# Performance work log

Hardware: AMD Instinct MI355X
Metric: run time of the kernel (lower is better)

## Reference

```python
import jax, jax.numpy as jnp
import numpy as np

TAU = 1.5
SCALE = 0.125
EPS = 1e-5
H = 8

@jax.custom_vjp
def spike(u):
    return (u >= 0.0).astype(u.dtype)

def _spike_fwd(u):
    return spike(u), u

def _spike_bwd(u, g):
    # ATan surrogate gradient, alpha=2 (spikingjelly default)
    return (g / (1.0 + (jnp.pi * u) ** 2),)

spike.defvjp(_spike_fwd, _spike_bwd)

def lif_ms(xt):
    # xt: (T, ...) multi-step LIF, decay_input=True, v_th=1, hard reset to 0, detach_reset
    def step(v, x):
        v = v + (x - v) / TAU
        s = spike(v - 1.0)
        v = v * (1.0 - jax.lax.stop_gradient(s))
        return v, s
    _, s = jax.lax.scan(step, jnp.zeros_like(xt[0]), xt)
    return s

def bn(x, g, b, m, var):
    # eval-mode BatchNorm1d over channel dim of (B, C, L)
    inv = g / jnp.sqrt(var + EPS)
    return (x - m[None, :, None]) * inv[None, :, None] + b[None, :, None]

def setup_inputs() -> dict:
    key = jax.random.key(0)
    ks = jax.random.split(key, 16)
    B, C, T, N = 8, 512, 4, 256
    w_scale = 1.0 / np.sqrt(C)
    inp = {
        'x': jax.random.normal(ks[0], (B, C, T, N), jnp.float32),
        'wq': jax.random.normal(ks[1], (C, C), jnp.float32) * w_scale,
        'wk': jax.random.normal(ks[2], (C, C), jnp.float32) * w_scale,
        'wv': jax.random.normal(ks[3], (C, C), jnp.float32) * w_scale,
        'wp': jax.random.normal(ks[4], (C, C), jnp.float32) * w_scale,
        'bp': jnp.zeros((C,), jnp.float32),
        'gq': jax.random.uniform(ks[5], (C,), jnp.float32, 0.5, 1.5),
        'bq': jax.random.uniform(ks[6], (C,), jnp.float32),
        'mq': jnp.zeros((C,), jnp.float32),
        'vq': jnp.ones((C,), jnp.float32),
        'gk': jax.random.uniform(ks[7], (C,), jnp.float32, 0.5, 1.5),
        'bk': jax.random.uniform(ks[8], (C,), jnp.float32),
        'mk': jnp.zeros((C,), jnp.float32),
        'vk': jnp.ones((C,), jnp.float32),
        'gv': jax.random.uniform(ks[9], (C,), jnp.float32, 0.5, 1.5),
        'bv': jax.random.uniform(ks[10], (C,), jnp.float32),
        'mv': jnp.zeros((C,), jnp.float32),
        'vv': jnp.ones((C,), jnp.float32),
        'gp': jax.random.uniform(ks[11], (C,), jnp.float32, 0.5, 1.5),
        'bpn': jax.random.uniform(ks[12], (C,), jnp.float32),
        'mp': jnp.zeros((C,), jnp.float32),
        'vp': jnp.ones((C,), jnp.float32),
    }
    return inp

def reference(x, wq, wk, wv, wp, bp, gq, bq, mq, vq, gk, bk, mk, vk,
              gv, bv, mv, vv, gp, bpn, mp, vp):
    B, C, T, N = x.shape
    L = T * N
    d = C // H

    # proj_bn then multi-step proj_lif over time dim
    xb = bn(x.reshape(B, C, L), gp, bpn, mp, vp).reshape(B, C, T, N)
    s0 = lif_ms(jnp.transpose(xb, (2, 0, 1, 3)))            # (T,B,C,N)
    x_for_qkv = jnp.transpose(s0, (1, 2, 0, 3)).reshape(B, C, L)  # (B,C,L)

    def qkv_branch(w, g, b_, m, v_):
        y = bn(jnp.einsum('oc,bcl->bol', w, x_for_qkv), g, b_, m, v_)
        y = y.reshape(B, C, T, N)
        sy = lif_ms(jnp.transpose(y, (2, 0, 1, 3)))         # (T,B,C,N)
        sy = jnp.transpose(sy, (1, 0, 3, 2)).reshape(B, L, C)  # (B,T,N,C)->(B,L,C)
        return jnp.transpose(sy.reshape(B, L, H, d), (0, 2, 1, 3))  # (B,H,L,d)

    q = qkv_branch(wq, gq, bq, mq, vq)
    k = qkv_branch(wk, gk, bk, mk, vk)
    v = qkv_branch(wv, gv, bv, mv, vv)

    attn = jnp.einsum('bhqd,bhkd->bhqk', q, k)              # no softmax
    o = jnp.einsum('bhqk,bhkd->bhqd', attn, v) * SCALE
    o = jnp.transpose(o, (0, 1, 3, 2)).reshape(B, C, L)

    # single-step attn_lif: v = o/tau from zero state, spike at threshold 1
    s = spike(o / TAU - 1.0)

    out = jnp.einsum('oc,bcl->bol', wp, s) + bp[None, :, None]
    return out.reshape(B, C, T, N)
```

## Files before the change

### kernel.cpp

```cpp
#include <hip/hip_runtime.h>
#include <hip/hip_bf16.h>


#define NB 8
#define NC 512
#define NT 4
#define NN 256
#define NL 1024
#define NH 8
#define ND 64
#define BCL (NB*NC*NL)

typedef __attribute__((ext_vector_type(8))) short  short8v;
typedef __attribute__((ext_vector_type(8))) unsigned short us8;
typedef __attribute__((ext_vector_type(4))) unsigned short us4;
typedef __attribute__((ext_vector_type(4))) float f32x4;

__device__ __forceinline__ float bu2f(unsigned short u) {
  return __uint_as_float(((unsigned)u) << 16);
}
__device__ __forceinline__ unsigned short f2bu(float f) {
  unsigned b = __float_as_uint(f);
  return (unsigned short)((b + 0x7FFFu + ((b >> 16) & 1u)) >> 16);
}

__global__ void k_prep(const float* __restrict__ wq, const float* __restrict__ wk,
                       const float* __restrict__ wv, const float* __restrict__ wp,
                       const float* __restrict__ x,
                       const float* __restrict__ g,  const float* __restrict__ bt,
                       const float* __restrict__ mu, const float* __restrict__ var,
                       unsigned short* __restrict__ H2,
                       unsigned short* __restrict__ ST0) {
  if (blockIdx.x < 512) {
    int gi = blockIdx.x * 256 + threadIdx.x;
    int p = gi >> 15;
    int o = (gi >> 6) & 511;
    int k8 = gi & 63;
    int rt = o >> 7, r = o & 127;
    int k0i = k8 >> 3, chunk = k8 & 7;
    const float* W = (p == 0) ? wq : (p == 1) ? wk : (p == 2) ? wv : wp;
    const float* src = W + (size_t)o * NC + k8 * 8;
    us8 a[3];
#pragma unroll
    for (int i = 0; i < 8; i++) {
      float w = src[i];
      unsigned short u1 = f2bu(w);
      float r1 = w - bu2f(u1);
      unsigned short u2 = f2bu(r1);
      float r2 = r1 - bu2f(u2);
      unsigned short u3 = f2bu(r2);
      a[0][i] = u1; a[1][i] = u2; a[2][i] = u3;
    }
#pragma unroll
    for (int j = 0; j < 3; j++) {
      size_t off = ((size_t)((((p * 3 + j) * 4 + rt) * 8 + k0i) * 8 + chunk)) * 1024
                   + (size_t)r * 8;
      *(us8*)&H2[off] = a[j];
    }
  } else {
    int bidx = blockIdx.x - 512;
    int b  = bidx >> 6;
    int c0 = (bidx & 63) * 8;
    int n  = threadIdx.x;
    unsigned short spk[NT][8];
#pragma unroll
    for (int i = 0; i < 8; i++) {
      int c = c0 + i;
      float inv = g[c] / sqrtf(var[c] + 1e-5f);
      float m = mu[c], be = bt[c];
      const float* xp = x + ((size_t)(b * NC + c)) * NL + n;
      float v = 0.f;
#pragma unroll
      for (int t = 0; t < NT; t++) {
        float y = (xp[t * NN] - m) * inv + be;
        v = v + (y - v) / 1.5f;
        unsigned short s = 0;
        if (v - 1.0f >= 0.f) { s = 0x3F80; v = 0.f; }
        spk[t][i] = s;
      }
    }
#pragma unroll
    for (int t = 0; t < NT; t++) {
      us8 pk;
#pragma unroll
      for (int i = 0; i < 8; i++) pk[i] = spk[t][i];
      *(us8*)&ST0[((size_t)b * NL + t * NN + n) * NC + c0] = pk;
    }
  }
}

__global__ __launch_bounds__(256) void
k_qkv(const unsigned short* __restrict__ H2,
      const unsigned short* __restrict__ ST0,
      const float* __restrict__ gq, const float* __restrict__ bq,
      const float* __restrict__ mq, const float* __restrict__ vq,
      const float* __restrict__ gk, const float* __restrict__ bk,
      const float* __restrict__ mk, const float* __restrict__ vk,
      const float* __restrict__ gv, const float* __restrict__ bv,
      const float* __restrict__ mv, const float* __restrict__ vv,
      unsigned short* __restrict__ STq, unsigned short* __restrict__ STkT,
      unsigned short* __restrict__ STvT) {
  __shared__ __align__(16) unsigned short sB[2][128 * 64];

  int id = blockIdx.x;
  int xcd = id & 7, slot = id >> 3;
  int b = xcd;
  int grp = slot >> 3;
  int p = grp >> 2, rt = grp & 3;
  int n0 = (slot & 7) * 32;

  int tid = threadIdx.x;
  int w = tid >> 6, lane = tid & 63, quad = lane >> 4, l15 = lane & 15;
  int xorv = l15 & 7;

  const unsigned short* Sb = ST0 + (size_t)b * NL * NC;
  const unsigned short* Hbase = H2 + ((size_t)((p * 3) * 4 + rt) * 8) * 8192;

  f32x4 acc[2][8];
#pragma unroll
  for (int ri = 0; ri < 2; ri++)
#pragma unroll
    for (int jj = 0; jj < 8; jj++) acc[ri][jj] = (f32x4){0.f, 0.f, 0.f, 0.f};

  short8v A0[2][3][2], A1[2][3][2];

#define QLOADA(DST, K0I)                                                     \
  _Pragma("unroll") for (int ks = 0; ks < 2; ks++) {                         \
    int c8 = ks * 4 + quad;                                                  \
    _Pragma("unroll") for (int j = 0; j < 3; j++) {                          \
      const unsigned short* Hj =                                             \
          Hbase + ((size_t)(j * 4 * 8 + (K0I))) * 8192 + (size_t)c8 * 1024;  \
      DST[ks][j][0] = *(const short8v*)&Hj[(w * 32 + l15) * 8];              \
      DST[ks][j][1] = *(const short8v*)&Hj[(w * 32 + 16 + l15) * 8];         \
    }                                                                        \
  }

  QLOADA(A0, 0);

  us8 breg[4];
  int ccs[4], segs[4];
  size_t bsrc[4];
#pragma unroll
  for (int i = 0; i < 4; i++) {
    int idx = tid + i * 256;
    int cc = idx >> 3, seg = idx & 7;
    int t = (cc >> 4) & 3, nn = (cc & 15) | ((cc >> 6) << 4);
    ccs[i] = cc; segs[i] = seg;
    bsrc[i] = (size_t)(t * NN + n0 + nn) * NC + seg * 8;
  }
#pragma unroll
  for (int i = 0; i < 4; i++) breg[i] = *(const us8*)&Sb[bsrc[i]];
#pragma unroll
  for (int i = 0; i < 4; i++)
    *(us8*)&sB[0][ccs[i] * 64 + ((segs[i] ^ (ccs[i] & 7)) << 3)] = breg[i];

#define QBPRE(K0N)                                                           \
  _Pragma("unroll") for (int i = 0; i < 4; i++)                              \
    breg[i] = *(const us8*)&Sb[bsrc[i] + (size_t)(K0N) * 64];

#define QBWRITE(BUFN)                                                        \
  _Pragma("unroll") for (int i = 0; i < 4; i++)                              \
    *(us8*)&sB[BUFN][ccs[i] * 64 + ((segs[i] ^ (ccs[i] & 7)) << 3)] = breg[i];

#define QMFMAS(AR, BUF)                                                      \
  _Pragma("unroll") for (int ks = 0; ks < 2; ks++) {                         \
    int c8 = ks * 4 + quad;                                                  \
    int poff = (c8 ^ xorv) << 3;                                             \
    short8v bf[8];                                                           \
    _Pragma("unroll") for (int jj = 0; jj < 8; jj++)                         \
      bf[jj] = *(const short8v*)&sB[BUF][(jj * 16 + l15) * 64 + poff];       \
    _Pragma("unroll") for (int j = 0; j < 3; j++)                            \
      _Pragma("unroll") for (int jj = 0; jj < 8; jj++) {                     \
        acc[0][jj] = __builtin_amdgcn_mfma_f32_16x16x32_bf16(                \
            AR[ks][j][0], bf[jj], acc[0][jj], 0, 0, 0);                      \
        acc[1][jj] = __builtin_amdgcn_mfma_f32_16x16x32_bf16(                \
            AR[ks][j][1], bf[jj], acc[1][jj], 0, 0, 0);                      \
      }                                                                      \
  }

#define QSTEP(K0I, ACUR, ANXT)                                               \
  __syncthreads();                                                           \
  { if ((K0I) < 7) { QLOADA(ANXT, (K0I) + 1); } }                            \
  { if ((K0I) < 7) { QBPRE((K0I) + 1); } }                                   \
  QMFMAS(ACUR, (K0I) & 1);                                                   \
  { if ((K0I) < 7) { QBWRITE(((K0I) & 1) ^ 1); } }

  QSTEP(0, A0, A1)
  QSTEP(1, A1, A0)
  QSTEP(2, A0, A1)
  QSTEP(3, A1, A0)
  QSTEP(4, A0, A1)
  QSTEP(5, A1, A0)
  QSTEP(6, A0, A1)
  QSTEP(7, A1, A0)

#undef QLOADA
#undef QBPRE
#undef QBWRITE
#undef QMFMAS
#undef QSTEP

  const float *g, *bb, *mpt, *vr;
  unsigned short* So;
  if (p == 0)      { g = gq; bb = bq; mpt = mq; vr = vq; So = STq; }
  else if (p == 1) { g = gk; bb = bk; mpt = mk; vr = vk; So = STkT; }
  else             { g = gv; bb = bv; mpt = mv; vr = vv; So = STvT; }
  So += (size_t)b * NL * NC;

  unsigned short spa[2][2][4][4];
#pragma unroll
  for (int ri = 0; ri < 2; ri++) {
    int ob = rt * 128 + w * 32 + ri * 16 + quad * 4;
    float av[4], mvv[4], bvv[4];
#pragma unroll
    for (int r = 0; r < 4; r++) {
      av[r]  = g[ob + r] / sqrtf(vr[ob + r] + 1e-5f);
      mvv[r] = mpt[ob + r];
      bvv[r] = bb[ob + r];
    }
#pragma unroll
    for (int nh = 0; nh < 2; nh++) {
#pragma unroll
      for (int r = 0; r < 4; r++) {
        float vmem = 0.f;
#pragma unroll
        for (int t = 0; t < NT; t++) {
          float y = (acc[ri][nh * 4 + t][r] - mvv[r]) * av[r] + bvv[r];
          vmem = vmem + (y - vmem) / 1.5f;
          unsigned short s = 0;
          if (vmem - 1.0f >= 0.f) { s = 0x3F80; vmem = 0.f; }
          spa[ri][nh][t][r] = s;
        }
      }
    }
  }

  __syncthreads();
  unsigned short* sT = &sB[0][0];

  if (p == 0) {
#pragma unroll
    for (int ri = 0; ri < 2; ri++)
#pragma unroll
      for (int nh = 0; nh < 2; nh++)
#pragma unroll
        for (int t = 0; t < 4; t++)
#pragma unroll
          for (int r = 0; r < 4; r++) {
            int lloc = t * 32 + (nh << 4) + l15;
            int col = w * 32 + ri * 16 + quad * 4 + r;
            int ch = col >> 3;
            int pch = (ch & 8) | ((ch & 7) ^ (lloc & 7));
            sT[lloc * 128 + (pch << 3) + (col & 7)] = spa[ri][nh][t][r];
          }
    __syncthreads();
#pragma unroll
    for (int ss = 0; ss < 2; ss++) {
      int s = tid + ss * 256;
      int lloc = s >> 2, seg = s & 3;
      int t = lloc >> 5, nn = lloc & 31;
      size_t rowg = (size_t)(t * NN + n0 + nn) * NC + rt * 128 + seg * 32;
#pragma unroll
      for (int i = 0; i < 4; i++) {
        int ch = seg * 4 + i;
        int pch = (ch & 8) | ((ch & 7) ^ (lloc & 7));
        us8 v = *(const us8*)&sT[lloc * 128 + (pch << 3)];
        *(us8*)&So[rowg + i * 8] = v;
      }
    }
  } else {
#pragma unroll
    for (int ri = 0; ri < 2; ri++)
#pragma unroll
      for (int nh = 0; nh < 2; nh++)
#pragma unroll
        for (int t = 0; t < 4; t++)
#pragma unroll
          for (int r = 0; r < 4; r++) {
            int row = w * 32 + ri * 16 + quad * 4 + r;
            int col = t * 32 + (nh << 4) + l15;
            int phys = (((col >> 3) ^ (row & 7)) << 3) | (col & 7);
            sT[row * 128 + phys] = spa[ri][nh][t][r];
          }
    __syncthreads();
#pragma unroll
    for (int ss = 0; ss < 2; ss++) {
      int s = tid + ss * 256;
      int c = s >> 2, t = s & 3;
#pragma unroll
      for (int i = 0; i < 4; i++) {
        int g8 = t * 4 + i;
        us8 v = *(const us8*)&sT[c * 128 + ((g8 ^ (c & 7)) << 3)];
        *(us8*)&So[(size_t)(rt * 128 + c) * NL + t * 256 + n0 + i * 8] = v;
      }
    }
  }
}

__global__ __launch_bounds__(256) void
k_kvM(const unsigned short* __restrict__ STkT,
      const unsigned short* __restrict__ STvT,
      float* __restrict__ Mpart) {
  int bh = blockIdx.x, ch = blockIdx.y;
  int b = bh >> 3, h = bh & 7;
  const unsigned short* KT = STkT + ((size_t)(b * NC + h * ND)) * NL;
  const unsigned short* VT = STvT + ((size_t)(b * NC + h * ND)) * NL;
  int tid = threadIdx.x;
  int w = tid >> 6, lane = tid & 63, quad = lane >> 4, l15 = lane & 15;
  int lb = ch * 128;

  f32x4 acc[4];
#pragma unroll
  for (int jj = 0; jj < 4; jj++) acc[jj] = (f32x4){0.f, 0.f, 0.f, 0.f};

#pragma unroll
  for (int ks = 0; ks < 4; ks++) {
    int lc = lb + ks * 32 + quad * 8;
    short8v a = *(const short8v*)&KT[(size_t)(w * 16 + l15) * NL + lc];
#pragma unroll
    for (int jj = 0; jj < 4; jj++) {
      short8v bv = *(const short8v*)&VT[(size_t)(jj * 16 + l15) * NL + lc];
      acc[jj] = __builtin_amdgcn_mfma_f32_16x16x32_bf16(a, bv, acc[jj], 0, 0, 0);
    }
  }

  float* Mp = Mpart + ((size_t)ch * 64 + bh) * 4096;
#pragma unroll
  for (int jj = 0; jj < 4; jj++)
#pragma unroll
    for (int r = 0; r < 4; r++)
      Mp[(w * 16 + quad * 4 + r) * ND + jj * 16 + l15] = acc[jj][r];
}

__global__ __launch_bounds__(256) void
k_red(const float* __restrict__ Mpart, float* __restrict__ Msum) {
  int i = blockIdx.x * 256 + threadIdx.x;
  float4 s = ((const float4*)Mpart)[i];
#pragma unroll
  for (int ch = 1; ch < 8; ch++) {
    float4 t = ((const float4*)Mpart)[(size_t)ch * 65536 + i];
    s.x += t.x; s.y += t.y; s.z += t.z; s.w += t.w;
  }
  ((float4*)Msum)[i] = s;
}

__global__ __launch_bounds__(256) void
k_attn(const unsigned short* __restrict__ STq,
       const float* __restrict__ Msum,
       unsigned short* __restrict__ STs) {
  __shared__ unsigned short MT1[64 * 64];
  __shared__ unsigned short MT2[64 * 64];
  __shared__ unsigned short sQ[128 * 64];
  int lt = blockIdx.x, bh = blockIdx.y;
  int b = bh >> 3, h = bh & 7;
  int tid = threadIdx.x;
  int w = tid >> 6, lane = tid & 63, quad = lane >> 4, l15 = lane & 15;

  const unsigned short* Qp = STq + (size_t)b * NL * NC + h * ND;

#pragma unroll
  for (int i = 0; i < 4; i++) {
    int idx = tid + i * 256;
    int row = idx >> 3, c8 = idx & 7;
    us8 v = *(const us8*)&Qp[(size_t)(lt * 128 + row) * NC + c8 * 8];
    *(us8*)&sQ[row * 64 + ((c8 ^ (row & 7)) << 3)] = v;
  }

#pragma unroll
  for (int i = 0; i < 4; i++) {
    int idx4 = tid + i * 256;
    float4 s = ((const float4*)Msum)[(size_t)bh * 1024 + idx4];
    int e = idx4 >> 4;
    int dd0 = (idx4 * 4) & 63;
    int chunk = e >> 3;
    float sv[4] = {s.x, s.y, s.z, s.w};
#pragma unroll
    for (int r = 0; r < 4; r++) {
      int dd = dd0 + r;
      unsigned short u1 = f2bu(sv[r]);
      unsigned short u2 = f2bu(sv[r] - bu2f(u1));
      int pos = dd * 64 + (((chunk ^ (dd & 7)) << 3) | (e & 7));
      MT1[pos] = u1;
      MT2[pos] = u2;
    }
  }
  __syncthreads();

  f32x4 acc[4][2];
#pragma unroll
  for (int dt = 0; dt < 4; dt++)
#pragma unroll
    for (int j = 0; j < 2; j++) acc[dt][j] = (f32x4){0.f, 0.f, 0.f, 0.f};

#pragma unroll
  for (int ks = 0; ks < 2; ks++) {
    short8v bq[2];
#pragma unroll
    for (int ltile = 0; ltile < 2; ltile++) {
      int row = w * 32 + ltile * 16 + l15;
      bq[ltile] = *(const short8v*)&sQ[row * 64
                                       + (((ks * 4 + quad) ^ (row & 7)) << 3)];
    }
    int c8 = ks * 4 + quad;
#pragma unroll
    for (int dt = 0; dt < 4; dt++) {
      int dd = dt * 16 + l15;
      int off = dd * 64 + ((c8 ^ (dd & 7)) << 3);
      short8v a1 = *(const short8v*)&MT1[off];
      short8v a2 = *(const short8v*)&MT2[off];
#pragma unroll
      for (int ltile = 0; ltile < 2; ltile++) {
        acc[dt][ltile] = __builtin_amdgcn_mfma_f32_16x16x32_bf16(a1, bq[ltile], acc[dt][ltile], 0, 0, 0);
        acc[dt][ltile] = __builtin_amdgcn_mfma_f32_16x16x32_bf16(a2, bq[ltile], acc[dt][ltile], 0, 0, 0);
      }
    }
  }

  __syncthreads();
#pragma unroll
  for (int dt = 0; dt < 4; dt++)
#pragma unroll
    for (int ltile = 0; ltile < 2; ltile++) {
      int row = w * 32 + ltile * 16 + l15;
#pragma unroll
      for (int r = 0; r < 4; r++) {
        int col = dt * 16 + quad * 4 + r;
        int phys = (((col >> 3) ^ (row & 7)) << 3) | (col & 7);
        sQ[row * 64 + phys] = (acc[dt][ltile][r] >= 12.0f) ? 0x3F80 : 0;
      }
    }
  __syncthreads();

  unsigned short* Sp = STs + (size_t)b * NL * NC + h * ND;
  {
    int row = tid >> 1, seg = tid & 1;
    size_t dst = (size_t)(lt * 128 + row) * NC + seg * 32;
#pragma unroll
    for (int i = 0; i < 4; i++) {
      int ch = seg * 4 + i;
      us8 v = *(const us8*)&sQ[row * 64 + ((ch ^ (row & 7)) << 3)];
      *(us8*)&Sp[dst + i * 8] = v;
    }
  }
}

__global__ __launch_bounds__(256) void
k_out(const unsigned short* __restrict__ H2,
      const unsigned short* __restrict__ STs,
      const float* __restrict__ bp, float* __restrict__ out) {
  __shared__ __align__(16) unsigned short sB[2][64 * 64];

  int id = blockIdx.x;
  int xcd = id & 7, slot = id >> 3;
  int b  = xcd;
  int rt = slot >> 4;
  int l0 = (slot & 15) * 64;

  int tid = threadIdx.x;
  int w = tid >> 6, lane = tid & 63, quad = lane >> 4, l15 = lane & 15;
  int xorv = l15 & 7;

  const unsigned short* Sb = STs + (size_t)b * NL * NC;
  const unsigned short* Hbase = H2 + ((size_t)(9 * 4 + rt) * 8) * 8192;

  f32x4 acc[2][4];
#pragma unroll
  for (int ri = 0; ri < 2; ri++)
#pragma unroll
    for (int jj = 0; jj < 4; jj++) acc[ri][jj] = (f32x4){0.f, 0.f, 0.f, 0.f};

  short8v A0[2][3][2], A1[2][3][2];

#define OLOADA(DST, K0I)                                                     \
  _Pragma("unroll") for (int ks = 0; ks < 2; ks++) {                         \
    int c8 = ks * 4 + quad;                                                  \
    _Pragma("unroll") for (int j = 0; j < 3; j++) {                          \
      const unsigned short* Hj =                                             \
          Hbase + ((size_t)(j * 4 * 8 + (K0I))) * 8192 + (size_t)c8 * 1024;  \
      DST[ks][j][0] = *(const short8v*)&Hj[(w * 32 + l15) * 8];              \
      DST[ks][j][1] = *(const short8v*)&Hj[(w * 32 + 16 + l15) * 8];         \
    }                                                                        \
  }

  OLOADA(A0, 0);

  us8 breg[2];
  int ccs[2], segs[2];
  size_t bsrc[2];
#pragma unroll
  for (int i = 0; i < 2; i++) {
    int idx = tid + i * 256;
    int cc = idx >> 3, seg = idx & 7;
    ccs[i] = cc; segs[i] = seg;
    bsrc[i] = (size_t)(l0 + cc) * NC + seg * 8;
  }
#pragma unroll
  for (int i = 0; i < 2; i++) breg[i] = *(const us8*)&Sb[bsrc[i]];
#pragma unroll
  for (int i = 0; i < 2; i++)
    *(us8*)&sB[0][ccs[i] * 64 + ((segs[i] ^ (ccs[i] & 7)) << 3)] = breg[i];

#define OBPRE(K0N)                                                           \
  _Pragma("unroll") for (int i = 0; i < 2; i++)                              \
    breg[i] = *(const us8*)&Sb[bsrc[i] + (size_t)(K0N) * 64];

#define OBWRITE(BUFN)                                                        \
  _Pragma("unroll") for (int i = 0; i < 2; i++)                              \
    *(us8*)&sB[BUFN][ccs[i] * 64 + ((segs[i] ^ (ccs[i] & 7)) << 3)] = breg[i];

#define OMFMAS(AR, BUF)                                                      \
  _Pragma("unroll") for (int ks = 0; ks < 2; ks++) {                         \
    int c8 = ks * 4 + quad;                                                  \
    int poff = (c8 ^ xorv) << 3;                                             \
    short8v bf[4];                                                           \
    _Pragma("unroll") for (int jj = 0; jj < 4; jj++)                         \
      bf[jj] = *(const short8v*)&sB[BUF][(jj * 16 + l15) * 64 + poff];       \
    _Pragma("unroll") for (int j = 0; j < 3; j++)                            \
      _Pragma("unroll") for (int jj = 0; jj < 4; jj++) {                     \
        acc[0][jj] = __builtin_amdgcn_mfma_f32_16x16x32_bf16(                \
            AR[ks][j][0], bf[jj], acc[0][jj], 0, 0, 0);                      \
        acc[1][jj] = __builtin_amdgcn_mfma_f32_16x16x32_bf16(                \
            AR[ks][j][1], bf[jj], acc[1][jj], 0, 0, 0);                      \
      }                                                                      \
  }

#define OSTEP(K0I, ACUR, ANXT)                                               \
  __syncthreads();                                                           \
  { if ((K0I) < 7) { OLOADA(ANXT, (K0I) + 1); } }                            \
  { if ((K0I) < 7) { OBPRE((K0I) + 1); } }                                   \
  OMFMAS(ACUR, (K0I) & 1);                                                   \
  { if ((K0I) < 7) { OBWRITE(((K0I) & 1) ^ 1); } }

  OSTEP(0, A0, A1)
  OSTEP(1, A1, A0)
  OSTEP(2, A0, A1)
  OSTEP(3, A1, A0)
  OSTEP(4, A0, A1)
  OSTEP(5, A1, A0)
  OSTEP(6, A0, A1)
  OSTEP(7, A1, A0)

#undef OLOADA
#undef OBPRE
#undef OBWRITE
#undef OMFMAS
#undef OSTEP

#pragma unroll
  for (int ri = 0; ri < 2; ri++) {
    int ob = rt * 128 + w * 32 + ri * 16 + quad * 4;
#pragma unroll
    for (int jj = 0; jj < 4; jj++) {
      int l = l0 + jj * 16 + l15;
#pragma unroll
      for (int r = 0; r < 4; r++)
        out[((size_t)(b * NC + ob + r)) * NL + l] = acc[ri][jj][r] + bp[ob + r];
    }
  }
}

extern "C" void kernel_launch(void* const* d_in, const int* in_sizes, int n_in,
                              void* d_out, int out_size, void* d_ws, size_t ws_size,
                              hipStream_t stream) {
  (void)in_sizes; (void)n_in; (void)out_size; (void)ws_size;
  const float* x   = (const float*)d_in[0];
  const float* wq  = (const float*)d_in[1];
  const float* wk  = (const float*)d_in[2];
  const float* wv  = (const float*)d_in[3];
  const float* wp  = (const float*)d_in[4];
  const float* bp  = (const float*)d_in[5];
  const float* gq  = (const float*)d_in[6];
  const float* bq  = (const float*)d_in[7];
  const float* mq  = (const float*)d_in[8];
  const float* vq  = (const float*)d_in[9];
  const float* gk  = (const float*)d_in[10];
  const float* bk  = (const float*)d_in[11];
  const float* mk  = (const float*)d_in[12];
  const float* vk  = (const float*)d_in[13];
  const float* gv  = (const float*)d_in[14];
  const float* bv  = (const float*)d_in[15];
  const float* mv  = (const float*)d_in[16];
  const float* vvv = (const float*)d_in[17];
  const float* gp  = (const float*)d_in[18];
  const float* bpn = (const float*)d_in[19];
  const float* mp  = (const float*)d_in[20];
  const float* vp  = (const float*)d_in[21];

  unsigned short* H2   = (unsigned short*)d_ws;
  unsigned short* ST0  = H2 + (size_t)4 * 3 * NC * NC;
  unsigned short* STq  = ST0 + BCL;
  unsigned short* STkT = STq + BCL;
  unsigned short* STvT = STkT + BCL;
  unsigned short* STs  = STvT + BCL;
  float* Mpart = (float*)(STs + BCL);
  float* Msum  = Mpart + (size_t)8 * 64 * 4096;

  dim3 blk(256);
  k_prep<<<1024, blk, 0, stream>>>(wq, wk, wv, wp, x, gp, bpn, mp, vp, H2, ST0);
  k_qkv<<<768, blk, 0, stream>>>(H2, ST0,
      gq, bq, mq, vq, gk, bk, mk, vk, gv, bv, mv, vvv, STq, STkT, STvT);
  k_kvM<<<dim3(64, 8), blk, 0, stream>>>(STkT, STvT, Mpart);
  k_red<<<256, blk, 0, stream>>>(Mpart, Msum);
  k_attn<<<dim3(8, 64), blk, 0, stream>>>(STq, Msum, STs);
  k_out<<<512, blk, 0, stream>>>(H2, STs, bp, (float*)d_out);
}
```

Baseline: 182.5 us.

## Replace triple-bf16 weight split with two-term fp16 split in projection GEMMs

Weights are now split into an fp16 high part and a residual scaled by 2^11, instead of three bf16 terms. Spikes are encoded as fp16 ones, and the GEMMs use f16 MFMA. The K loop runs twice, residual term first, with the accumulator rescaled by 2^-11 before the high term is added. This removes a third of the MFMA work and weight loads. It restructures the loop to stream one weight term per pass, which re-reads the B tiles from global memory and LDS twice and doubles the number of barriers. The fp16 range and precision of the split weights could differ slightly from the fp32 reference, which matters near spike thresholds.

```diff
diff --git a/kernel.cpp b/kernel.cpp
--- a/kernel.cpp
+++ b/kernel.cpp
@@ -12,6 +12,7 @@
 #define BCL (NB*NC*NL)
 
 typedef __attribute__((ext_vector_type(8))) short  short8v;
+typedef __attribute__((ext_vector_type(8))) _Float16 h8;
 typedef __attribute__((ext_vector_type(8))) unsigned short us8;
 typedef __attribute__((ext_vector_type(4))) unsigned short us4;
 typedef __attribute__((ext_vector_type(4))) float f32x4;
@@ -40,20 +41,19 @@
     int k0i = k8 >> 3, chunk = k8 & 7;
     const float* W = (p == 0) ? wq : (p == 1) ? wk : (p == 2) ? wv : wp;
     const float* src = W + (size_t)o * NC + k8 * 8;
-    us8 a[3];
+    us8 a[2];
 #pragma unroll
     for (int i = 0; i < 8; i++) {
       float w = src[i];
-      unsigned short u1 = f2bu(w);
-      float r1 = w - bu2f(u1);
-      unsigned short u2 = f2bu(r1);
-      float r2 = r1 - bu2f(u2);
-      unsigned short u3 = f2bu(r2);
-      a[0][i] = u1; a[1][i] = u2; a[2][i] = u3;
-    }
-#pragma unroll
-    for (int j = 0; j < 3; j++) {
-      size_t off = ((size_t)((((p * 3 + j) * 4 + rt) * 8 + k0i) * 8 + chunk)) * 1024
+      _Float16 h1 = (_Float16)w;
+      float r1 = w - (float)h1;
+      _Float16 h2 = (_Float16)(r1 * 2048.0f);
+      a[0][i] = __builtin_bit_cast(unsigned short, h1);
+      a[1][i] = __builtin_bit_cast(unsigned short, h2);
+    }
+#pragma unroll
+    for (int j = 0; j < 2; j++) {
+      size_t off = ((size_t)((((p * 2 + j) * 4 + rt) * 8 + k0i) * 8 + chunk)) * 1024
                    + (size_t)r * 8;
       *(us8*)&H2[off] = a[j];
     }
@@ -75,7 +75,7 @@
         float y = (xp[t * NN] - m) * inv + be;
         v = v + (y - v) / 1.5f;
         unsigned short s = 0;
-        if (v - 1.0f >= 0.f) { s = 0x3F80; v = 0.f; }
+        if (v - 1.0f >= 0.f) { s = 0x3C00; v = 0.f; }
         spk[t][i] = s;
       }
     }
@@ -114,7 +114,7 @@
   int xorv = l15 & 7;
 
   const unsigned short* Sb = ST0 + (size_t)b * NL * NC;
-  const unsigned short* Hbase = H2 + ((size_t)((p * 3) * 4 + rt) * 8) * 8192;
+  const unsigned short* Hbase = H2 + ((size_t)((p * 2) * 4 + rt) * 8) * 8192;
 
   f32x4 acc[2][8];
 #pragma unroll
@@ -122,20 +122,18 @@
 #pragma unroll
     for (int jj = 0; jj < 8; jj++) acc[ri][jj] = (f32x4){0.f, 0.f, 0.f, 0.f};
 
-  short8v A0[2][3][2], A1[2][3][2];
-
-#define QLOADA(DST, K0I)                                                     \
+  h8 A0[2][2], A1[2][2];
+
+#define QLOADA(DST, J, K0I)                                                  \
   _Pragma("unroll") for (int ks = 0; ks < 2; ks++) {                         \
     int c8 = ks * 4 + quad;                                                  \
-    _Pragma("unroll") for (int j = 0; j < 3; j++) {                          \
-      const unsigned short* Hj =                                             \
-          Hbase + ((size_t)(j * 4 * 8 + (K0I))) * 8192 + (size_t)c8 * 1024;  \
-      DST[ks][j][0] = *(const short8v*)&Hj[(w * 32 + l15) * 8];              \
-      DST[ks][j][1] = *(const short8v*)&Hj[(w * 32 + 16 + l15) * 8];         \
-    }                                                                        \
-  }
-
-  QLOADA(A0, 0);
+    const unsigned short* Hj =                                               \
+        Hbase + ((size_t)((J) * 4 * 8 + (K0I))) * 8192 + (size_t)c8 * 1024;  \
+    DST[ks][0] = *(const h8*)&Hj[(w * 32 + l15) * 8];                        \
+    DST[ks][1] = *(const h8*)&Hj[(w * 32 + 16 + l15) * 8];                   \
+  }
+
+  QLOADA(A0, 1, 0);
 
   us8 breg[4];
   int ccs[4], segs[4];
@@ -166,33 +164,44 @@
   _Pragma("unroll") for (int ks = 0; ks < 2; ks++) {                         \
     int c8 = ks * 4 + quad;                                                  \
     int poff = (c8 ^ xorv) << 3;                                             \
-    short8v bf[8];                                                           \
-    _Pragma("unroll") for (int jj = 0; jj < 8; jj++)                         \
-      bf[jj] = *(const short8v*)&sB[BUF][(jj * 16 + l15) * 64 + poff];       \
-    _Pragma("unroll") for (int j = 0; j < 3; j++)                            \
-      _Pragma("unroll") for (int jj = 0; jj < 8; jj++) {                     \
-        acc[0][jj] = __builtin_amdgcn_mfma_f32_16x16x32_bf16(                \
-            AR[ks][j][0], bf[jj], acc[0][jj], 0, 0, 0);                      \
-        acc[1][jj] = __builtin_amdgcn_mfma_f32_16x16x32_bf16(                \
-            AR[ks][j][1], bf[jj], acc[1][jj], 0, 0, 0);                      \
-      }                                                                      \
-  }
-
-#define QSTEP(K0I, ACUR, ANXT)                                               \
+    _Pragma("unroll") for (int jj = 0; jj < 8; jj++) {                       \
+      h8 bf = *(const h8*)&sB[BUF][(jj * 16 + l15) * 64 + poff];             \
+      acc[0][jj] = __builtin_amdgcn_mfma_f32_16x16x32_f16(                   \
+          AR[ks][0], bf, acc[0][jj], 0, 0, 0);                               \
+      acc[1][jj] = __builtin_amdgcn_mfma_f32_16x16x32_f16(                   \
+          AR[ks][1], bf, acc[1][jj], 0, 0, 0);                               \
+    }                                                                        \
+  }
+
+#define QSTEP(S, ACUR, ANXT, JN, KN)                                         \
   __syncthreads();                                                           \
-  { if ((K0I) < 7) { QLOADA(ANXT, (K0I) + 1); } }                            \
-  { if ((K0I) < 7) { QBPRE((K0I) + 1); } }                                   \
-  QMFMAS(ACUR, (K0I) & 1);                                                   \
-  { if ((K0I) < 7) { QBWRITE(((K0I) & 1) ^ 1); } }
-
-  QSTEP(0, A0, A1)
-  QSTEP(1, A1, A0)
-  QSTEP(2, A0, A1)
-  QSTEP(3, A1, A0)
-  QSTEP(4, A0, A1)
-  QSTEP(5, A1, A0)
-  QSTEP(6, A0, A1)
-  QSTEP(7, A1, A0)
+  { if ((S) < 15) { QLOADA(ANXT, JN, KN); } }                                \
+  { if ((S) < 15) { QBPRE(KN); } }                                           \
+  QMFMAS(ACUR, (S) & 1);                                                     \
+  { if ((S) < 15) { QBWRITE(((S) & 1) ^ 1); } }
+
+  QSTEP(0,  A0, A1, 1, 1)
+  QSTEP(1,  A1, A0, 1, 2)
+  QSTEP(2,  A0, A1, 1, 3)
+  QSTEP(3,  A1, A0, 1, 4)
+  QSTEP(4,  A0, A1, 1, 5)
+  QSTEP(5,  A1, A0, 1, 6)
+  QSTEP(6,  A0, A1, 1, 7)
+  QSTEP(7,  A1, A0, 0, 0)
+#pragma unroll
+  for (int ri = 0; ri < 2; ri++)
+#pragma unroll
+    for (int jj = 0; jj < 8; jj++)
+#pragma unroll
+      for (int r = 0; r < 4; r++) acc[ri][jj][r] *= 0x1p-11f;
+  QSTEP(8,  A0, A1, 0, 1)
+  QSTEP(9,  A1, A0, 0, 2)
+  QSTEP(10, A0, A1, 0, 3)
+  QSTEP(11, A1, A0, 0, 4)
+  QSTEP(12, A0, A1, 0, 5)
+  QSTEP(13, A1, A0, 0, 6)
+  QSTEP(14, A0, A1, 0, 7)
+  QSTEP(15, A1, A0, 0, 0)
 
 #undef QLOADA
 #undef QBPRE
@@ -426,7 +435,7 @@
       for (int r = 0; r < 4; r++) {
         int col = dt * 16 + quad * 4 + r;
         int phys = (((col >> 3) ^ (row & 7)) << 3) | (col & 7);
-        sQ[row * 64 + phys] = (acc[dt][ltile][r] >= 12.0f) ? 0x3F80 : 0;
+        sQ[row * 64 + phys] = (acc[dt][ltile][r] >= 12.0f) ? 0x3C00 : 0;
       }
     }
   __syncthreads();
@@ -461,7 +470,7 @@
   int xorv = l15 & 7;
 
   const unsigned short* Sb = STs + (size_t)b * NL * NC;
-  const unsigned short* Hbase = H2 + ((size_t)(9 * 4 + rt) * 8) * 8192;
+  const unsigned short* Hbase = H2 + ((size_t)((3 * 2) * 4 + rt) * 8) * 8192;
 
   f32x4 acc[2][4];
 #pragma unroll
@@ -469,20 +478,18 @@
 #pragma unroll
     for (int jj = 0; jj < 4; jj++) acc[ri][jj] = (f32x4){0.f, 0.f, 0.f, 0.f};
 
-  short8v A0[2][3][2], A1[2][3][2];
-
-#define OLOADA(DST, K0I)                                                     \
+  h8 A0[2][2], A1[2][2];
+
+#define OLOADA(DST, J, K0I)                                                  \
   _Pragma("unroll") for (int ks = 0; ks < 2; ks++) {                         \
     int c8 = ks * 4 + quad;                                                  \
-    _Pragma("unroll") for (int j = 0; j < 3; j++) {                          \
-      const unsigned short* Hj =                                             \
-          Hbase + ((size_t)(j * 4 * 8 + (K0I))) * 8192 + (size_t)c8 * 1024;  \
-      DST[ks][j][0] = *(const short8v*)&Hj[(w * 32 + l15) * 8];              \
-      DST[ks][j][1] = *(const short8v*)&Hj[(w * 32 + 16 + l15) * 8];         \
-    }                                                                        \
-  }
-
-  OLOADA(A0, 0);
+    const unsigned short* Hj =                                               \
+        Hbase + ((size_t)((J) * 4 * 8 + (K0I))) * 8192 + (size_t)c8 * 1024;  \
+    DST[ks][0] = *(const h8*)&Hj[(w * 32 + l15) * 8];                        \
+    DST[ks][1] = *(const h8*)&Hj[(w * 32 + 16 + l15) * 8];                   \
+  }
+
+  OLOADA(A0, 1, 0);
 
   us8 breg[2];
   int ccs[2], segs[2];
@@ -512,33 +519,44 @@
   _Pragma("unroll") for (int ks = 0; ks < 2; ks++) {                         \
     int c8 = ks * 4 + quad;                                                  \
     int poff = (c8 ^ xorv) << 3;                                             \
-    short8v bf[4];                                                           \
-    _Pragma("unroll") for (int jj = 0; jj < 4; jj++)                         \
-      bf[jj] = *(const short8v*)&sB[BUF][(jj * 16 + l15) * 64 + poff];       \
-    _Pragma("unroll") for (int j = 0; j < 3; j++)                            \
-      _Pragma("unroll") for (int jj = 0; jj < 4; jj++) {                     \
-        acc[0][jj] = __builtin_amdgcn_mfma_f32_16x16x32_bf16(                \
-            AR[ks][j][0], bf[jj], acc[0][jj], 0, 0, 0);                      \
-        acc[1][jj] = __builtin_amdgcn_mfma_f32_16x16x32_bf16(                \
-            AR[ks][j][1], bf[jj], acc[1][jj], 0, 0, 0);                      \
-      }                                                                      \
-  }
-
-#define OSTEP(K0I, ACUR, ANXT)                                               \
+    _Pragma("unroll") for (int jj = 0; jj < 4; jj++) {                       \
+      h8 bf = *(const h8*)&sB[BUF][(jj * 16 + l15) * 64 + poff];             \
+      acc[0][jj] = __builtin_amdgcn_mfma_f32_16x16x32_f16(                   \
+          AR[ks][0], bf, acc[0][jj], 0, 0, 0);                               \
+      acc[1][jj] = __builtin_amdgcn_mfma_f32_16x16x32_f16(                   \
+          AR[ks][1], bf, acc[1][jj], 0, 0, 0);                               \
+    }                                                                        \
+  }
+
+#define OSTEP(S, ACUR, ANXT, JN, KN)                                         \
   __syncthreads();                                                           \
-  { if ((K0I) < 7) { OLOADA(ANXT, (K0I) + 1); } }                            \
-  { if ((K0I) < 7) { OBPRE((K0I) + 1); } }                                   \
-  OMFMAS(ACUR, (K0I) & 1);                                                   \
-  { if ((K0I) < 7) { OBWRITE(((K0I) & 1) ^ 1); } }
-
-  OSTEP(0, A0, A1)
-  OSTEP(1, A1, A0)
-  OSTEP(2, A0, A1)
-  OSTEP(3, A1, A0)
-  OSTEP(4, A0, A1)
-  OSTEP(5, A1, A0)
-  OSTEP(6, A0, A1)
-  OSTEP(7, A1, A0)
+  { if ((S) < 15) { OLOADA(ANXT, JN, KN); } }                                \
+  { if ((S) < 15) { OBPRE(KN); } }                                           \
+  OMFMAS(ACUR, (S) & 1);                                                     \
+  { if ((S) < 15) { OBWRITE(((S) & 1) ^ 1); } }
+
+  OSTEP(0,  A0, A1, 1, 1)
+  OSTEP(1,  A1, A0, 1, 2)
+  OSTEP(2,  A0, A1, 1, 3)
+  OSTEP(3,  A1, A0, 1, 4)
+  OSTEP(4,  A0, A1, 1, 5)
+  OSTEP(5,  A1, A0, 1, 6)
+  OSTEP(6,  A0, A1, 1, 7)
+  OSTEP(7,  A1, A0, 0, 0)
+#pragma unroll
+  for (int ri = 0; ri < 2; ri++)
+#pragma unroll
+    for (int jj = 0; jj < 4; jj++)
+#pragma unroll
+      for (int r = 0; r < 4; r++) acc[ri][jj][r] *= 0x1p-11f;
+  OSTEP(8,  A0, A1, 0, 1)
+  OSTEP(9,  A1, A0, 0, 2)
+  OSTEP(10, A0, A1, 0, 3)
+  OSTEP(11, A1, A0, 0, 4)
+  OSTEP(12, A0, A1, 0, 5)
+  OSTEP(13, A1, A0, 0, 6)
+  OSTEP(14, A0, A1, 0, 7)
+  OSTEP(15, A1, A0, 0, 0)
 
 #undef OLOADA
 #undef OBPRE
```

Result: slower. 189.5 us (+3.9%).
